# Optimization experiments

Measured on AMD Instinct MI355X. Metric: run time of the kernel, lower is better.

The kernel has to match this reference:

```python
import jax, jax.numpy as jnp
import numpy as np

PAD = 20  # (41 - 1) // 2, matches ReflectionPad2d(20)
CHANNELS = 6


def _matlab_gauss2d(shape=(41, 41), sigma=10.0):
    m, n = [(s - 1.0) / 2.0 for s in shape]
    y, x = np.ogrid[-m:m + 1, -n:n + 1]
    h = np.exp(-(x * x + y * y) / (2.0 * sigma * sigma))
    h[h < np.finfo(h.dtype).eps * h.max()] = 0
    s = h.sum()
    if s != 0:
        h /= s
    return h


def setup_inputs() -> dict:
    key = jax.random.key(0)
    x = jax.random.normal(key, (16, CHANNELS, 512, 512), dtype=jnp.float32)
    k = _matlab_gauss2d((41, 41), 10.0)  # [41, 41]
    # depthwise weight [C, 1, 41, 41], same kernel repeated per channel
    weight = jnp.asarray(np.repeat(k[None, None], CHANNELS, axis=0), dtype=jnp.float32)
    return {"x": x, "weight": weight}


def reference(x, weight):
    # reflect-pad H and W by 20 (PyTorch ReflectionPad2d semantics == jnp 'reflect')
    xp = jnp.pad(x, ((0, 0), (0, 0), (PAD, PAD), (PAD, PAD)), mode="reflect")
    # depthwise conv: feature_group_count = C, weight is [C, 1, kH, kW]
    out = jax.lax.conv_general_dilated(
        xp, weight,
        window_strides=(1, 1),
        padding="VALID",
        dimension_numbers=("NCHW", "OIHW", "NCHW"),
        feature_group_count=CHANNELS,
    )
    return out  # [B, C, H, W]
```

## Files before the change

kernel.cpp:

```cpp
#include <hip/hip_runtime.h>

#define KS 41
#define PAD 20
#define H 512
#define W 512
#define CH 6

__device__ __forceinline__ int reflect_idx(int i, int n) {
    if (i < 0) i = -i;
    if (i >= n) i = 2 * n - 2 - i;
    return i;
}

__device__ __forceinline__ int reflect511(int i) {
    return (H - 1) - abs((H - 1) - abs(i));
}

__device__ __forceinline__ float uniform_f(float v) {
    return __uint_as_float(__builtin_amdgcn_readfirstlane(__float_as_uint(v)));
}

__global__ __launch_bounds__(256, 4)
void gauss_h_kernel(const float* __restrict__ x, const float* __restrict__ w,
                    float* __restrict__ ws) {
    __shared__ float g_s[KS];
    __shared__ float rowbuf[4][576];

    const int tid = threadIdx.x;
    const int wv = tid >> 6;
    const int l  = tid & 63;
    const int img = blockIdx.y;
    const int c   = img % CH;
    const int row = blockIdx.x * 4 + wv;

    if (tid < KS) {
        const float* wr = w + (size_t)c * KS * KS + (size_t)tid * KS;
        float s = 0.f;
        #pragma unroll
        for (int j = 0; j < KS; ++j) s += wr[j];
        g_s[tid] = s;
    }

    const float4* src4 = (const float4*)(x + ((size_t)img * H + row) * W);
    float4 v0 = src4[l];
    float4 v1 = src4[l + 64];
    float* L = rowbuf[wv];
    *(float4*)(L + PAD + 4 * l)       = v0;
    *(float4*)(L + PAD + 256 + 4 * l) = v1;
    __syncthreads();

    if (l < 2 * PAD) {
        const int dst  = (l < PAD) ? l        : (W + l);
        const int srcp = (l < PAD) ? (40 - l) : (550 - l);
        float hv = L[srcp];
        L[dst] = hv;
    }
    __syncthreads();

    float gk[KS];
    #pragma unroll
    for (int j = 0; j < KS; ++j) gk[j] = uniform_f(g_s[j]);

    float* dst = ws + ((size_t)img * H + row) * W;
    #pragma unroll
    for (int k = 0; k < 2; ++k) {
        const int x0 = 256 * k + 4 * l;
        float win[44];
        #pragma unroll
        for (int m = 0; m < 11; ++m) {
            float4 q = *(const float4*)(L + x0 + 4 * m);
            win[4 * m + 0] = q.x; win[4 * m + 1] = q.y;
            win[4 * m + 2] = q.z; win[4 * m + 3] = q.w;
        }
        float a0 = 0.f, a1 = 0.f, a2 = 0.f, a3 = 0.f;
        #pragma unroll
        for (int j = 0; j < KS; ++j) {
            const float gj = gk[j];
            a0 += gj * win[j + 0];
            a1 += gj * win[j + 1];
            a2 += gj * win[j + 2];
            a3 += gj * win[j + 3];
        }
        *(float4*)(dst + x0) = make_float4(a0, a1, a2, a3);
    }
}

__global__ __launch_bounds__(256, 4)
void gauss_v_kernel(const float* __restrict__ ws, const float* __restrict__ w,
                    float* __restrict__ out) {
    __shared__ float g_s[KS];
    const int tid = threadIdx.x;
    const int img = blockIdx.y;
    const int c   = img % CH;
    const int y0  = blockIdx.x * 16;

    if (tid < KS) {
        const float* wr = w + (size_t)c * KS * KS + (size_t)tid * KS;
        float s = 0.f;
        #pragma unroll
        for (int j = 0; j < KS; ++j) s += wr[j];
        g_s[tid] = s;
    }
    __syncthreads();

    float gk[KS];
    #pragma unroll
    for (int j = 0; j < KS; ++j) gk[j] = uniform_f(g_s[j]);

    const float* sbase = ws + (size_t)img * H * W + 2 * tid;
    float* obase = out + ((size_t)img * H + y0) * W + 2 * tid;

    float2 acc[16];
    #pragma unroll
    for (int r = 0; r < 16; ++r) acc[r] = make_float2(0.f, 0.f);

    #pragma unroll
    for (int i = 0; i < 56; ++i) {
        const int rr = reflect511(y0 - PAD + i);
        const float2 v = *(const float2*)(sbase + (size_t)rr * W);
        #pragma unroll
        for (int r = 0; r < 16; ++r) {
            const int j = i - r;
            if (j >= 0 && j < KS) {
                acc[r].x += gk[j] * v.x;
                acc[r].y += gk[j] * v.y;
            }
        }
    }
    #pragma unroll
    for (int r = 0; r < 16; ++r)
        *((float2*)(obase + (size_t)r * W)) = acc[r];
}

#define TW 64
#define TH 128
#define TMPH (TH + 2 * PAD)

__global__ __launch_bounds__(256, 3)
void gauss_blur_fused_kernel(const float* __restrict__ x,
                             const float* __restrict__ w,
                             float* __restrict__ out) {
    __shared__ float g_s[KS];
    __shared__ float tmp[TMPH * TW];

    const int tid = threadIdx.x;
    const int bx = blockIdx.x, by = blockIdx.y, bz = blockIdx.z;
    const int c = bz % CH;

    if (tid < KS) {
        const float* wr = w + (size_t)c * KS * KS + (size_t)tid * KS;
        float s = 0.f;
        #pragma unroll
        for (int j = 0; j < KS; ++j) s += wr[j];
        g_s[tid] = s;
    }
    __syncthreads();

    float gr[KS];
    #pragma unroll
    for (int j = 0; j < KS; ++j) gr[j] = uniform_f(g_s[j]);

    const size_t img_off = (size_t)bz * (H * W);
    const float* img = x + img_off;
    const int x_tile = bx * TW;

    for (int gid = tid; gid < TMPH * (TW / 8); gid += 256) {
        const int r  = gid >> 3;
        const int gx = gid & 7;
        const int gy = reflect_idx(by * TH - PAD + r, H);
        const int x0 = x_tile + gx * 8;
        const float* row = img + (size_t)gy * W;

        float buf[48];
        if (x0 >= PAD && x0 + 27 <= W - 1) {
            const float4* p = (const float4*)(row + x0 - PAD);
            #pragma unroll
            for (int m = 0; m < 12; ++m) {
                float4 v = p[m];
                buf[4 * m + 0] = v.x; buf[4 * m + 1] = v.y;
                buf[4 * m + 2] = v.z; buf[4 * m + 3] = v.w;
            }
        } else {
            #pragma unroll
            for (int j = 0; j < 48; ++j)
                buf[j] = row[reflect_idx(x0 - PAD + j, W)];
        }

        float s[8];
        #pragma unroll
        for (int k = 0; k < 8; ++k) s[k] = 0.f;
        #pragma unroll
        for (int j = 0; j < KS; ++j) {
            #pragma unroll
            for (int k = 0; k < 8; ++k) s[k] += gr[j] * buf[j + k];
        }
        float* dstp = &tmp[r * TW + gx * 8];
        #pragma unroll
        for (int k = 0; k < 8; ++k) dstp[k] = s[k];
    }
    __syncthreads();

    const int lx = tid & 63;
    const int yg = tid >> 6;
    float* o = out + img_off;

    #pragma unroll
    for (int cc = 0; cc < 2; ++cc) {
        const int yc = yg * 32 + cc * 16;
        float col[56];
        #pragma unroll
        for (int i = 0; i < 56; ++i)
            col[i] = tmp[(yc + i) * TW + lx];
        #pragma unroll
        for (int y = 0; y < 16; ++y) {
            float s = 0.f;
            #pragma unroll
            for (int j = 0; j < KS; ++j) s += gr[j] * col[y + j];
            o[(size_t)(by * TH + yc + y) * W + x_tile + lx] = s;
        }
    }
}

extern "C" void kernel_launch(void* const* d_in, const int* in_sizes, int n_in,
                              void* d_out, int out_size, void* d_ws, size_t ws_size,
                              hipStream_t stream) {
    const float* x = (const float*)d_in[0];
    const float* w = (const float*)d_in[1];
    float* out = (float*)d_out;
    (void)in_sizes; (void)n_in; (void)out_size;

    const size_t need = (size_t)16 * CH * H * W * sizeof(float);
    if (ws_size >= need) {
        float* ws = (float*)d_ws;
        gauss_h_kernel<<<dim3(H / 4, 16 * CH), 256, 0, stream>>>(x, w, ws);
        gauss_v_kernel<<<dim3(H / 16, 16 * CH), 256, 0, stream>>>(ws, w, out);
    } else {
        dim3 grid(W / TW, H / TH, 16 * CH);
        gauss_blur_fused_kernel<<<grid, 256, 0, stream>>>(x, w, out);
    }
}
```

Baseline: 263.5 us.

## Rework separable blur: per-wave LDS rows with swizzle, LDS-tiled vertical pass

The horizontal pass now computes the 1D coefficients per wave through readlane instead of a shared-memory array and block barrier. Each wave handles one row with wave-local barriers, an XOR-swizzled LDS layout and 8 outputs per lane. The vertical pass becomes a 64x128 tile that stages 168 rows of the intermediate into LDS, so each thread reuses a column window instead of issuing strided float2 global loads. The intent is to cut block-level synchronisation, LDS bank conflicts and redundant global traffic, at the cost of higher LDS usage and register pressure in the vertical kernel.

```diff
diff --git a/kernel.cpp b/kernel.cpp
--- a/kernel.cpp
+++ b/kernel.cpp
@@ -20,116 +20,132 @@
     return __uint_as_float(__builtin_amdgcn_readfirstlane(__float_as_uint(v)));
 }
 
+__device__ __forceinline__ void load_coeffs(const float* __restrict__ w, int c,
+                                            int lane, float gk[KS]) {
+    float my = 0.f;
+    if (lane < KS) {
+        const float* wr = w + (size_t)c * KS * KS + (size_t)lane * KS;
+        #pragma unroll
+        for (int j = 0; j < KS; ++j) my += wr[j];
+    }
+    #pragma unroll
+    for (int j = 0; j < KS; ++j)
+        gk[j] = __uint_as_float(__builtin_amdgcn_readlane(__float_as_uint(my), j));
+}
+
+__device__ __forceinline__ void st4_swz(float* L, int q, float4 v) {
+    const int pq = q ^ ((q >> 3) & 7);
+    *(float4*)(L + 4 * pq) = v;
+}
+__device__ __forceinline__ float4 ld4_swz(const float* L, int q) {
+    const int pq = q ^ ((q >> 3) & 7);
+    return *(const float4*)(L + 4 * pq);
+}
+__device__ __forceinline__ int swz(int p) {
+    return p ^ (((p >> 5) & 7) << 2);
+}
+
 __global__ __launch_bounds__(256, 4)
 void gauss_h_kernel(const float* __restrict__ x, const float* __restrict__ w,
                     float* __restrict__ ws) {
-    __shared__ float g_s[KS];
-    __shared__ float rowbuf[4][576];
+    __shared__ float rowbuf[4][560];
 
     const int tid = threadIdx.x;
-    const int wv = tid >> 6;
-    const int l  = tid & 63;
+    const int wv  = tid >> 6;
+    const int l   = tid & 63;
     const int img = blockIdx.y;
     const int c   = img % CH;
     const int row = blockIdx.x * 4 + wv;
 
-    if (tid < KS) {
-        const float* wr = w + (size_t)c * KS * KS + (size_t)tid * KS;
-        float s = 0.f;
-        #pragma unroll
-        for (int j = 0; j < KS; ++j) s += wr[j];
-        g_s[tid] = s;
-    }
+    float gk[KS];
+    load_coeffs(w, c, l, gk);
 
     const float4* src4 = (const float4*)(x + ((size_t)img * H + row) * W);
     float4 v0 = src4[l];
     float4 v1 = src4[l + 64];
     float* L = rowbuf[wv];
-    *(float4*)(L + PAD + 4 * l)       = v0;
-    *(float4*)(L + PAD + 256 + 4 * l) = v1;
-    __syncthreads();
+    st4_swz(L, l + 5, v0);
+    st4_swz(L, l + 69, v1);
+    __builtin_amdgcn_wave_barrier();
 
     if (l < 2 * PAD) {
-        const int dst  = (l < PAD) ? l        : (W + l);
+        const int dstp = (l < PAD) ? l        : (512 + l);
         const int srcp = (l < PAD) ? (40 - l) : (550 - l);
-        float hv = L[srcp];
-        L[dst] = hv;
-    }
-    __syncthreads();
-
-    float gk[KS];
-    #pragma unroll
-    for (int j = 0; j < KS; ++j) gk[j] = uniform_f(g_s[j]);
-
-    float* dst = ws + ((size_t)img * H + row) * W;
-    #pragma unroll
-    for (int k = 0; k < 2; ++k) {
-        const int x0 = 256 * k + 4 * l;
-        float win[44];
-        #pragma unroll
-        for (int m = 0; m < 11; ++m) {
-            float4 q = *(const float4*)(L + x0 + 4 * m);
-            win[4 * m + 0] = q.x; win[4 * m + 1] = q.y;
-            win[4 * m + 2] = q.z; win[4 * m + 3] = q.w;
-        }
-        float a0 = 0.f, a1 = 0.f, a2 = 0.f, a3 = 0.f;
-        #pragma unroll
-        for (int j = 0; j < KS; ++j) {
-            const float gj = gk[j];
-            a0 += gj * win[j + 0];
-            a1 += gj * win[j + 1];
-            a2 += gj * win[j + 2];
-            a3 += gj * win[j + 3];
-        }
-        *(float4*)(dst + x0) = make_float4(a0, a1, a2, a3);
-    }
-}
-
-__global__ __launch_bounds__(256, 4)
+        float hv = L[swz(srcp)];
+        L[swz(dstp)] = hv;
+    }
+    __builtin_amdgcn_wave_barrier();
+
+    float win[48];
+    #pragma unroll
+    for (int m = 0; m < 12; ++m) {
+        float4 q = ld4_swz(L, 2 * l + m);
+        win[4 * m + 0] = q.x; win[4 * m + 1] = q.y;
+        win[4 * m + 2] = q.z; win[4 * m + 3] = q.w;
+    }
+
+    float acc[8];
+    #pragma unroll
+    for (int i = 0; i < 8; ++i) acc[i] = 0.f;
+    #pragma unroll
+    for (int j = 0; j < KS; ++j) {
+        const float gj = gk[j];
+        #pragma unroll
+        for (int i = 0; i < 8; ++i) acc[i] += gj * win[j + i];
+    }
+
+    float* dst = ws + ((size_t)img * H + row) * W + 8 * l;
+    *(float4*)(dst)     = make_float4(acc[0], acc[1], acc[2], acc[3]);
+    *(float4*)(dst + 4) = make_float4(acc[4], acc[5], acc[6], acc[7]);
+}
+
+#define VTW 64
+#define VTH 128
+#define VTMPH (VTH + 2 * PAD)
+
+__global__ __launch_bounds__(256, 3)
 void gauss_v_kernel(const float* __restrict__ ws, const float* __restrict__ w,
                     float* __restrict__ out) {
-    __shared__ float g_s[KS];
+    __shared__ float tmp[VTMPH * VTW];
+
     const int tid = threadIdx.x;
-    const int img = blockIdx.y;
+    const int bx  = blockIdx.x;
+    const int by  = blockIdx.y;
+    const int img = blockIdx.z;
     const int c   = img % CH;
-    const int y0  = blockIdx.x * 16;
-
-    if (tid < KS) {
-        const float* wr = w + (size_t)c * KS * KS + (size_t)tid * KS;
-        float s = 0.f;
-        #pragma unroll
-        for (int j = 0; j < KS; ++j) s += wr[j];
-        g_s[tid] = s;
+
+    float gk[KS];
+    load_coeffs(w, c, tid & 63, gk);
+
+    const float* sbase = ws + (size_t)img * H * W + bx * VTW;
+    for (int idx = tid; idx < VTMPH * 16; idx += 256) {
+        const int r  = idx >> 4;
+        const int q  = idx & 15;
+        const int sr = reflect511(by * VTH - PAD + r);
+        float4 v = *(const float4*)(sbase + (size_t)sr * W + 4 * q);
+        *(float4*)&tmp[r * VTW + 4 * q] = v;
     }
     __syncthreads();
 
-    float gk[KS];
-    #pragma unroll
-    for (int j = 0; j < KS; ++j) gk[j] = uniform_f(g_s[j]);
-
-    const float* sbase = ws + (size_t)img * H * W + 2 * tid;
-    float* obase = out + ((size_t)img * H + y0) * W + 2 * tid;
-
-    float2 acc[16];
-    #pragma unroll
-    for (int r = 0; r < 16; ++r) acc[r] = make_float2(0.f, 0.f);
-
-    #pragma unroll
-    for (int i = 0; i < 56; ++i) {
-        const int rr = reflect511(y0 - PAD + i);
-        const float2 v = *(const float2*)(sbase + (size_t)rr * W);
-        #pragma unroll
-        for (int r = 0; r < 16; ++r) {
-            const int j = i - r;
-            if (j >= 0 && j < KS) {
-                acc[r].x += gk[j] * v.x;
-                acc[r].y += gk[j] * v.y;
-            }
-        }
-    }
-    #pragma unroll
-    for (int r = 0; r < 16; ++r)
-        *((float2*)(obase + (size_t)r * W)) = acc[r];
+    const int lx = tid & 63;
+    const int yg = tid >> 6;
+    float* o = out + ((size_t)img * H + by * VTH) * W + bx * VTW + lx;
+
+    #pragma unroll
+    for (int cc = 0; cc < 2; ++cc) {
+        const int yc = yg * 32 + cc * 16;
+        float col[56];
+        #pragma unroll
+        for (int i = 0; i < 56; ++i)
+            col[i] = tmp[(yc + i) * VTW + lx];
+        #pragma unroll
+        for (int y = 0; y < 16; ++y) {
+            float s = 0.f;
+            #pragma unroll
+            for (int j = 0; j < KS; ++j) s += gk[j] * col[y + j];
+            o[(size_t)(yc + y) * W] = s;
+        }
+    }
 }
 
 #define TW 64
@@ -233,7 +249,7 @@
     if (ws_size >= need) {
         float* ws = (float*)d_ws;
         gauss_h_kernel<<<dim3(H / 4, 16 * CH), 256, 0, stream>>>(x, w, ws);
-        gauss_v_kernel<<<dim3(H / 16, 16 * CH), 256, 0, stream>>>(ws, w, out);
+        gauss_v_kernel<<<dim3(W / VTW, H / VTH, 16 * CH), 256, 0, stream>>>(ws, w, out);
     } else {
         dim3 grid(W / TW, H / TH, 16 * CH);
         gauss_blur_fused_kernel<<<grid, 256, 0, stream>>>(x, w, out);
```

Result: faster. 243.4 us (-7.6%).
